# Kernel optimization log

Hardware: AMD Instinct MI355X
Metric: run time of the kernel (lower is better)

The kernel has to match this reference:

```python
import jax, jax.numpy as jnp
import numpy as np


def setup_inputs() -> dict:
    key = jax.random.key(0)
    ks = jax.random.split(key, 6)
    B, C, S = 256, 2048, 7          # batch, embed_dim, spacial_dim
    OUT = 1024                      # output_dim
    return {
        "x": jax.random.normal(ks[0], (B, C, S, S), jnp.float32),
        "pos_emb": jax.random.normal(ks[1], (S * S + 1, C), jnp.float32) / (C ** 0.5),
        "Wv": jax.random.normal(ks[2], (C, C), jnp.float32) * 0.02,
        "bv": jnp.zeros((C,), jnp.float32),
        "Wc": jax.random.normal(ks[3], (OUT, C), jnp.float32) * 0.02,
        "bc": jnp.zeros((OUT,), jnp.float32),
        "num_heads": 32,
    }


def reference(x, pos_emb, Wv, bv, Wc, bc, num_heads):
    # x: [B, C, H, W] -> tokens [B, HW, C], prepend mean token -> [B, N, C]
    B, C, H, W = x.shape
    N = H * W + 1
    hd = C // num_heads
    scale = hd ** -0.5

    t = x.reshape(B, C, H * W).transpose(0, 2, 1)                    # [B, HW, C]
    t = jnp.concatenate([t.mean(axis=1, keepdims=True), t], axis=1)  # [B, N, C]
    t = t + pos_emb[None]                                            # add pos emb

    # qkv weights are all copies of v_proj => q = k = v = v_proj(t)
    v = t @ Wv.T + bv                                                # [B, N, C]
    vh = v.reshape(B, N, num_heads, hd).transpose(0, 2, 1, 3)        # [B, h, N, d]

    # attn_ori = softmax(q k^T * scale) with q=k=v; dropout p=0 (eval)
    attn = jax.nn.softmax(jnp.einsum('bhnd,bhmd->bhnm', vh, vh) * scale, axis=-1)
    ctx = jnp.einsum('bhnm,bhmd->bhnd', attn, vh)                    # [B, h, N, d]
    ctx = ctx.transpose(0, 2, 1, 3).reshape(B, N, C)

    # proj weights come from c_proj: [out_dim, C]
    x_ori = ctx @ Wc.T + bc                                          # [B, N, out]
    xout = v @ Wc.T + bc                                             # x-path: proj(v) directly
    # x[:, 0, :] = x_ori[:, 0, :]; module returns x (first list element)
    return xout.at[:, 0, :].set(x_ori[:, 0, :])
```

## Files before the change

### kernel.cpp

```cpp
#include <hip/hip_runtime.h>
#include <stdint.h>

#define BATCH  256
#define CDIM   2048
#define HW     49
#define NTOK   50
#define MROWS  (BATCH * NTOK)
#define ODIM   1024
#define NHEADS 32

typedef __attribute__((ext_vector_type(8))) short short8;
typedef __attribute__((ext_vector_type(4))) float f32x4;
typedef unsigned short u16;
typedef unsigned int   u32;

__device__ __forceinline__ float bf2f(u16 u) {
  union { u32 i; float f; } v; v.i = ((u32)u) << 16; return v.f;
}
__device__ __forceinline__ u16 f2bf(float f) {
  union { float f; u32 i; } v; v.f = f;
  u32 r = v.i + 0x7fffu + ((v.i >> 16) & 1u);
  return (u16)(r >> 16);
}

__device__ __forceinline__ void async16(const void* g, void* l) {
  __builtin_amdgcn_global_load_lds(
      (const __attribute__((address_space(1))) u32*)g,
      (__attribute__((address_space(3))) u32*)l, 16, 0, 0);
}

__global__ __launch_bounds__(256) void cvt2_kernel(const float* __restrict__ a,
                                                   u16* __restrict__ oa, int n4a,
                                                   const float* __restrict__ bsrc,
                                                   u16* __restrict__ ob, int n4b) {
  int i = blockIdx.x * 256 + threadIdx.x;
  const float* src; u16* dst; int idx;
  if (i < n4a) { src = a; dst = oa; idx = i; }
  else {
    idx = i - n4a;
    if (idx >= n4b) return;
    src = bsrc; dst = ob;
  }
  float4 v = reinterpret_cast<const float4*>(src)[idx];
  ushort4 o;
  o.x = f2bf(v.x); o.y = f2bf(v.y); o.z = f2bf(v.z); o.w = f2bf(v.w);
  reinterpret_cast<ushort4*>(dst)[idx] = o;
}

__global__ __launch_bounds__(256) void prep_kernel(const float* __restrict__ x,
                                                   const float* __restrict__ pos,
                                                   u16* __restrict__ T) {
  const int blk = blockIdx.x;
  const int b  = blk >> 5;
  const int c0 = (blk & 31) * 64;
  __shared__ float xs[64 * HW];
  __shared__ float mean[64];
  const float* src = x + ((size_t)b * CDIM + c0) * HW;
  for (int i = threadIdx.x; i < 64 * HW; i += 256) xs[i] = src[i];
  __syncthreads();
  if (threadIdx.x < 64) {
    float s = 0.f;
#pragma unroll
    for (int j = 0; j < HW; j++) s += xs[threadIdx.x * HW + j];
    mean[threadIdx.x] = s * (1.0f / 49.0f);
  }
  __syncthreads();
  for (int wi = threadIdx.x; wi < NTOK * 8; wi += 256) {
    const int n = wi >> 3;
    const int g = (wi & 7) * 8;
    alignas(16) u16 ov[8];
#pragma unroll
    for (int u = 0; u < 8; u++) {
      const int c = g + u;
      float val = (n == 0) ? mean[c] : xs[c * HW + (n - 1)];
      val += pos[n * CDIM + c0 + c];
      ov[u] = f2bf(val);
    }
    *reinterpret_cast<uint4*>(&T[((size_t)b * NTOK + n) * CDIM + c0 + g]) =
        *reinterpret_cast<const uint4*>(ov);
  }
}

template<int OUT_BF16>
__global__ __launch_bounds__(512, 2)
void gemm256(const u16* __restrict__ A, const u16* __restrict__ Bm,
             const float* __restrict__ bias, void* __restrict__ Cout,
             int M, int N, int K, int nbx) {
  __shared__ __align__(16) u16 smem[65536];

  const int NK = K >> 6;
  const int t = threadIdx.x;
  const int lane = t & 63;
  const int wid = t >> 6;
  const int wm = wid >> 2;
  const int wn = wid & 3;

  const int nwg = gridDim.x;
  const int cpx = nwg >> 3;
  const int orig = blockIdx.x;
  const int swz = (orig & 7) * cpx + (orig >> 3);
  const int bx = swz % nbx;
  const int by = swz / nbx;
  const int m0 = by * 256, n0 = bx * 256;

  const int tr  = t >> 3;
  const int to8 = ((t & 7) ^ (tr & 7)) << 3;
  const int t8  = t << 3;
  const u16* pA0 = A  + (size_t)(m0 + tr) * K + to8;
  const u16* pB0 = Bm + (size_t)(n0 + tr) * K + to8;

  const int lr = lane & 15, hi = lane >> 4;
  const int sx = lr & 7;
  const int aK0 = ((wm * 128 + lr) << 6) + (((0 + hi) ^ sx) << 3);
  const int aK1 = ((wm * 128 + lr) << 6) + (((4 + hi) ^ sx) << 3);
  const int bK0 = 16384 + ((wn * 64 + lr) << 6) + (((0 + hi) ^ sx) << 3);
  const int bK1 = 16384 + ((wn * 64 + lr) << 6) + (((4 + hi) ^ sx) << 3);

  f32x4 acc[8][4] = {};
  short8 a[4][2], b[2][2];

  auto STG = [&](int kti, int isB, int h) {
    if (kti < NK) {
      const u16* g = (isB ? pB0 : pA0) + (size_t)(h * 128) * K + kti * 64;
      u16* l = &smem[((kti & 1) << 15) + (isB << 14) + (h << 13) + t8];
      async16(g, l);
      async16(g + (size_t)64 * K, l + 4096);
    }
  };

  STG(0, 0, 0); STG(0, 0, 1); STG(0, 1, 0); STG(0, 1, 1); STG(1, 0, 0);
  asm volatile("s_waitcnt vmcnt(2)" ::: "memory");
  __builtin_amdgcn_s_barrier();

  for (int j = 0; j < NK; ++j) {
    const u16* sa = &smem[(j & 1) << 15];

#pragma unroll
    for (int f = 0; f < 4; ++f) {
      a[f][0] = *(const short8*)&sa[aK0 + f * 1024];
      a[f][1] = *(const short8*)&sa[aK1 + f * 1024];
    }
#pragma unroll
    for (int f = 0; f < 2; ++f) {
      b[f][0] = *(const short8*)&sa[bK0 + f * 1024];
      b[f][1] = *(const short8*)&sa[bK1 + f * 1024];
    }
    STG(j + 1, 0, 1);
    __builtin_amdgcn_s_barrier();
    asm volatile("s_waitcnt lgkmcnt(0)" ::: "memory");
    __builtin_amdgcn_sched_barrier(0);
    __builtin_amdgcn_s_setprio(1);
#pragma unroll
    for (int fm = 0; fm < 4; ++fm)
#pragma unroll
      for (int fn = 0; fn < 2; ++fn) {
        acc[fm][fn] = __builtin_amdgcn_mfma_f32_16x16x32_bf16(a[fm][0], b[fn][0], acc[fm][fn], 0, 0, 0);
        acc[fm][fn] = __builtin_amdgcn_mfma_f32_16x16x32_bf16(a[fm][1], b[fn][1], acc[fm][fn], 0, 0, 0);
      }
    __builtin_amdgcn_s_setprio(0);
    __builtin_amdgcn_s_barrier();

#pragma unroll
    for (int f = 0; f < 2; ++f) {
      b[f][0] = *(const short8*)&sa[bK0 + (2 + f) * 1024];
      b[f][1] = *(const short8*)&sa[bK1 + (2 + f) * 1024];
    }
    STG(j + 1, 1, 0);
    __builtin_amdgcn_s_barrier();
    asm volatile("s_waitcnt lgkmcnt(0)" ::: "memory");
    __builtin_amdgcn_sched_barrier(0);
    __builtin_amdgcn_s_setprio(1);
#pragma unroll
    for (int fm = 0; fm < 4; ++fm)
#pragma unroll
      for (int fn = 0; fn < 2; ++fn) {
        acc[fm][2 + fn] = __builtin_amdgcn_mfma_f32_16x16x32_bf16(a[fm][0], b[fn][0], acc[fm][2 + fn], 0, 0, 0);
        acc[fm][2 + fn] = __builtin_amdgcn_mfma_f32_16x16x32_bf16(a[fm][1], b[fn][1], acc[fm][2 + fn], 0, 0, 0);
      }
    __builtin_amdgcn_s_setprio(0);
    __builtin_amdgcn_s_barrier();

#pragma unroll
    for (int f = 0; f < 4; ++f) {
      a[f][0] = *(const short8*)&sa[aK0 + (4 + f) * 1024];
      a[f][1] = *(const short8*)&sa[aK1 + (4 + f) * 1024];
    }
    STG(j + 1, 1, 1);
    __builtin_amdgcn_s_barrier();
    asm volatile("s_waitcnt lgkmcnt(0)" ::: "memory");
    __builtin_amdgcn_sched_barrier(0);
    __builtin_amdgcn_s_setprio(1);
#pragma unroll
    for (int fm = 0; fm < 4; ++fm)
#pragma unroll
      for (int fn = 0; fn < 2; ++fn) {
        acc[4 + fm][2 + fn] = __builtin_amdgcn_mfma_f32_16x16x32_bf16(a[fm][0], b[fn][0], acc[4 + fm][2 + fn], 0, 0, 0);
        acc[4 + fm][2 + fn] = __builtin_amdgcn_mfma_f32_16x16x32_bf16(a[fm][1], b[fn][1], acc[4 + fm][2 + fn], 0, 0, 0);
      }
    __builtin_amdgcn_s_setprio(0);
    __builtin_amdgcn_s_barrier();

#pragma unroll
    for (int f = 0; f < 2; ++f) {
      b[f][0] = *(const short8*)&sa[bK0 + f * 1024];
      b[f][1] = *(const short8*)&sa[bK1 + f * 1024];
    }
    STG(j + 2, 0, 0);
    __builtin_amdgcn_s_barrier();
    asm volatile("s_waitcnt lgkmcnt(0)" ::: "memory");
    __builtin_amdgcn_sched_barrier(0);
    __builtin_amdgcn_s_setprio(1);
#pragma unroll
    for (int fm = 0; fm < 4; ++fm)
#pragma unroll
      for (int fn = 0; fn < 2; ++fn) {
        acc[4 + fm][fn] = __builtin_amdgcn_mfma_f32_16x16x32_bf16(a[fm][0], b[fn][0], acc[4 + fm][fn], 0, 0, 0);
        acc[4 + fm][fn] = __builtin_amdgcn_mfma_f32_16x16x32_bf16(a[fm][1], b[fn][1], acc[4 + fm][fn], 0, 0, 0);
      }
    __builtin_amdgcn_s_setprio(0);
    if (j < NK - 2) asm volatile("s_waitcnt vmcnt(2)" ::: "memory");
    else            asm volatile("s_waitcnt vmcnt(0)" ::: "memory");
    __builtin_amdgcn_s_barrier();
  }

  const int erow = hi * 4;
#pragma unroll
  for (int fm = 0; fm < 8; ++fm) {
#pragma unroll
    for (int fn = 0; fn < 4; ++fn) {
      const int cg = n0 + wn * 64 + fn * 16 + lr;
      const float bb = bias[cg];
      const int rbase = m0 + wm * 128 + fm * 16 + erow;
#pragma unroll
      for (int jr = 0; jr < 4; ++jr) {
        const float val = acc[fm][fn][jr] + bb;
        if (OUT_BF16)
          ((u16*)Cout)[(size_t)(rbase + jr) * N + cg] = f2bf(val);
        else
          ((float*)Cout)[(size_t)(rbase + jr) * N + cg] = val;
      }
    }
  }
}

__global__ __launch_bounds__(64) void attn0_kernel(u16* __restrict__ V) {
  const int b = blockIdx.x, h = blockIdx.y;
  __shared__ __align__(16) u16 vt[NTOK * 64];
  __shared__ float pb[64];
  const int t = threadIdx.x;
  u16* base = V + (size_t)b * NTOK * CDIM + h * 64;
  for (int idx = t; idx < NTOK * 8; idx += 64) {
    const int m = idx >> 3, g = (idx & 7) * 8;
    *reinterpret_cast<uint4*>(&vt[m * 64 + g]) =
        *reinterpret_cast<const uint4*>(base + (size_t)m * CDIM + g);
  }
  __syncthreads();
  const float qd = bf2f(vt[t]);
  float s_own = -1e30f;
  for (int m = 0; m < NTOK; m++) {
    float p = qd * bf2f(vt[m * 64 + t]);
#pragma unroll
    for (int off = 32; off; off >>= 1) p += __shfl_xor(p, off);
    if (t == m) s_own = p * 0.125f;
  }
  float mx = s_own;
#pragma unroll
  for (int off = 32; off; off >>= 1) mx = fmaxf(mx, __shfl_xor(mx, off));
  const float e = (t < NTOK) ? __expf(s_own - mx) : 0.f;
  float Z = e;
#pragma unroll
  for (int off = 32; off; off >>= 1) Z += __shfl_xor(Z, off);
  pb[t] = e / Z;
  __syncthreads();
  float acc = 0.f;
  for (int m = 0; m < NTOK; m++) acc += pb[m] * bf2f(vt[m * 64 + t]);
  base[t] = f2bf(acc);
}

extern "C" void kernel_launch(void* const* d_in, const int* in_sizes, int n_in,
                              void* d_out, int out_size, void* d_ws, size_t ws_size,
                              hipStream_t stream) {
  const float* x   = (const float*)d_in[0];
  const float* pos = (const float*)d_in[1];
  const float* Wv  = (const float*)d_in[2];
  const float* bv  = (const float*)d_in[3];
  const float* Wc  = (const float*)d_in[4];
  const float* bc  = (const float*)d_in[5];
  float* out = (float*)d_out;

  u16* T   = (u16*)d_ws;
  u16* V   = T   + (size_t)MROWS * CDIM;
  u16* WvB = V   + (size_t)MROWS * CDIM;
  u16* WcB = WvB + (size_t)CDIM * CDIM;

  {
    int n4a = CDIM * CDIM / 4;
    int n4b = ODIM * CDIM / 4;
    cvt2_kernel<<<(n4a + n4b + 255) / 256, 256, 0, stream>>>(Wv, WvB, n4a, Wc, WcB, n4b);
  }
  prep_kernel<<<BATCH * 32, 256, 0, stream>>>(x, pos, T);

  gemm256<1><<<(MROWS / 256) * (CDIM / 256), 512, 0, stream>>>(
      T, WvB, bv, V, MROWS, CDIM, CDIM, CDIM / 256);

  attn0_kernel<<<dim3(BATCH, NHEADS), 64, 0, stream>>>(V);

  gemm256<0><<<(MROWS / 256) * (ODIM / 256), 512, 0, stream>>>(
      V, WcB, bc, out, MROWS, ODIM, CDIM, ODIM / 256);
}
```

Before: 310.5 us.

## Fuse weight conversion with prep kernel and restructure GEMM k-loop staging

```diff
diff --git a/kernel.cpp b/kernel.cpp
--- a/kernel.cpp
+++ b/kernel.cpp
@@ -29,34 +29,36 @@
       (__attribute__((address_space(3))) u32*)l, 16, 0, 0);
 }
 
-__global__ __launch_bounds__(256) void cvt2_kernel(const float* __restrict__ a,
-                                                   u16* __restrict__ oa, int n4a,
-                                                   const float* __restrict__ bsrc,
-                                                   u16* __restrict__ ob, int n4b) {
-  int i = blockIdx.x * 256 + threadIdx.x;
-  const float* src; u16* dst; int idx;
-  if (i < n4a) { src = a; dst = oa; idx = i; }
-  else {
-    idx = i - n4a;
-    if (idx >= n4b) return;
-    src = bsrc; dst = ob;
-  }
-  float4 v = reinterpret_cast<const float4*>(src)[idx];
-  ushort4 o;
-  o.x = f2bf(v.x); o.y = f2bf(v.y); o.z = f2bf(v.z); o.w = f2bf(v.w);
-  reinterpret_cast<ushort4*>(dst)[idx] = o;
-}
-
-__global__ __launch_bounds__(256) void prep_kernel(const float* __restrict__ x,
-                                                   const float* __restrict__ pos,
-                                                   u16* __restrict__ T) {
-  const int blk = blockIdx.x;
+#define BARRIER() asm volatile("s_barrier" ::: "memory")
+
+__global__ __launch_bounds__(256) void cvt_prep_kernel(
+    const float* __restrict__ Wv, u16* __restrict__ WvB, int n4a,
+    const float* __restrict__ Wc, u16* __restrict__ WcB, int n4b,
+    const float* __restrict__ x, const float* __restrict__ pos,
+    u16* __restrict__ T, int nCvt) {
+  if (blockIdx.x < (unsigned)nCvt) {
+    int i = blockIdx.x * 256 + threadIdx.x;
+    const float* src; u16* dst; int idx;
+    if (i < n4a) { src = Wv; dst = WvB; idx = i; }
+    else {
+      idx = i - n4a;
+      if (idx >= n4b) return;
+      src = Wc; dst = WcB;
+    }
+    float4 v = reinterpret_cast<const float4*>(src)[idx];
+    ushort4 o;
+    o.x = f2bf(v.x); o.y = f2bf(v.y); o.z = f2bf(v.z); o.w = f2bf(v.w);
+    reinterpret_cast<ushort4*>(dst)[idx] = o;
+    return;
+  }
+  const int blk = blockIdx.x - nCvt;
   const int b  = blk >> 5;
   const int c0 = (blk & 31) * 64;
   __shared__ float xs[64 * HW];
   __shared__ float mean[64];
   const float* src = x + ((size_t)b * CDIM + c0) * HW;
-  for (int i = threadIdx.x; i < 64 * HW; i += 256) xs[i] = src[i];
+  for (int i = threadIdx.x; i < 64 * HW / 4; i += 256)
+    reinterpret_cast<float4*>(xs)[i] = reinterpret_cast<const float4*>(src)[i];
   __syncthreads();
   if (threadIdx.x < 64) {
     float s = 0.f;
@@ -117,7 +119,7 @@
   const int bK1 = 16384 + ((wn * 64 + lr) << 6) + (((4 + hi) ^ sx) << 3);
 
   f32x4 acc[8][4] = {};
-  short8 a[4][2], b[2][2];
+  short8 a[4][2], b[4][2];
 
   auto STG = [&](int kti, int isB, int h) {
     if (kti < NK) {
@@ -128,9 +130,21 @@
     }
   };
 
-  STG(0, 0, 0); STG(0, 0, 1); STG(0, 1, 0); STG(0, 1, 1); STG(1, 0, 0);
-  asm volatile("s_waitcnt vmcnt(2)" ::: "memory");
-  __builtin_amdgcn_s_barrier();
+#define MFMA4x2(AM, BN0, ACCM, ACCN)                                          \
+  _Pragma("unroll")                                                           \
+  for (int fm = 0; fm < 4; ++fm) {                                            \
+    _Pragma("unroll")                                                         \
+    for (int fn = 0; fn < 2; ++fn) {                                          \
+      acc[(ACCM) + fm][(ACCN) + fn] = __builtin_amdgcn_mfma_f32_16x16x32_bf16(\
+          a[fm][0], b[(BN0) + fn][0], acc[(ACCM) + fm][(ACCN) + fn], 0, 0, 0);\
+      acc[(ACCM) + fm][(ACCN) + fn] = __builtin_amdgcn_mfma_f32_16x16x32_bf16(\
+          a[fm][1], b[(BN0) + fn][1], acc[(ACCM) + fm][(ACCN) + fn], 0, 0, 0);\
+    }                                                                         \
+  }
+
+  STG(0, 0, 0); STG(0, 0, 1); STG(0, 1, 0); STG(0, 1, 1);
+  asm volatile("s_waitcnt vmcnt(0)" ::: "memory");
+  BARRIER();
 
   for (int j = 0; j < NK; ++j) {
     const u16* sa = &smem[(j & 1) << 15];
@@ -145,82 +159,46 @@
       b[f][0] = *(const short8*)&sa[bK0 + f * 1024];
       b[f][1] = *(const short8*)&sa[bK1 + f * 1024];
     }
-    STG(j + 1, 0, 1);
-    __builtin_amdgcn_s_barrier();
+    STG(j + 1, 0, 0); STG(j + 1, 0, 1); STG(j + 1, 1, 0); STG(j + 1, 1, 1);
+    BARRIER();
     asm volatile("s_waitcnt lgkmcnt(0)" ::: "memory");
     __builtin_amdgcn_sched_barrier(0);
     __builtin_amdgcn_s_setprio(1);
-#pragma unroll
-    for (int fm = 0; fm < 4; ++fm)
-#pragma unroll
-      for (int fn = 0; fn < 2; ++fn) {
-        acc[fm][fn] = __builtin_amdgcn_mfma_f32_16x16x32_bf16(a[fm][0], b[fn][0], acc[fm][fn], 0, 0, 0);
-        acc[fm][fn] = __builtin_amdgcn_mfma_f32_16x16x32_bf16(a[fm][1], b[fn][1], acc[fm][fn], 0, 0, 0);
-      }
-    __builtin_amdgcn_s_setprio(0);
-    __builtin_amdgcn_s_barrier();
-
-#pragma unroll
-    for (int f = 0; f < 2; ++f) {
-      b[f][0] = *(const short8*)&sa[bK0 + (2 + f) * 1024];
-      b[f][1] = *(const short8*)&sa[bK1 + (2 + f) * 1024];
-    }
-    STG(j + 1, 1, 0);
-    __builtin_amdgcn_s_barrier();
+    MFMA4x2(lo, 0, 0, 0);
+    __builtin_amdgcn_s_setprio(0);
+    BARRIER();
+
+#pragma unroll
+    for (int f = 2; f < 4; ++f) {
+      b[f][0] = *(const short8*)&sa[bK0 + f * 1024];
+      b[f][1] = *(const short8*)&sa[bK1 + f * 1024];
+    }
+    BARRIER();
     asm volatile("s_waitcnt lgkmcnt(0)" ::: "memory");
     __builtin_amdgcn_sched_barrier(0);
     __builtin_amdgcn_s_setprio(1);
-#pragma unroll
-    for (int fm = 0; fm < 4; ++fm)
-#pragma unroll
-      for (int fn = 0; fn < 2; ++fn) {
-        acc[fm][2 + fn] = __builtin_amdgcn_mfma_f32_16x16x32_bf16(a[fm][0], b[fn][0], acc[fm][2 + fn], 0, 0, 0);
-        acc[fm][2 + fn] = __builtin_amdgcn_mfma_f32_16x16x32_bf16(a[fm][1], b[fn][1], acc[fm][2 + fn], 0, 0, 0);
-      }
-    __builtin_amdgcn_s_setprio(0);
-    __builtin_amdgcn_s_barrier();
+    MFMA4x2(lo, 2, 0, 2);
+    __builtin_amdgcn_s_setprio(0);
+    BARRIER();
 
 #pragma unroll
     for (int f = 0; f < 4; ++f) {
       a[f][0] = *(const short8*)&sa[aK0 + (4 + f) * 1024];
       a[f][1] = *(const short8*)&sa[aK1 + (4 + f) * 1024];
     }
-    STG(j + 1, 1, 1);
-    __builtin_amdgcn_s_barrier();
+    BARRIER();
     asm volatile("s_waitcnt lgkmcnt(0)" ::: "memory");
     __builtin_amdgcn_sched_barrier(0);
     __builtin_amdgcn_s_setprio(1);
-#pragma unroll
-    for (int fm = 0; fm < 4; ++fm)
-#pragma unroll
-      for (int fn = 0; fn < 2; ++fn) {
-        acc[4 + fm][2 + fn] = __builtin_amdgcn_mfma_f32_16x16x32_bf16(a[fm][0], b[fn][0], acc[4 + fm][2 + fn], 0, 0, 0);
-        acc[4 + fm][2 + fn] = __builtin_amdgcn_mfma_f32_16x16x32_bf16(a[fm][1], b[fn][1], acc[4 + fm][2 + fn], 0, 0, 0);
-      }
-    __builtin_amdgcn_s_setprio(0);
-    __builtin_amdgcn_s_barrier();
-
-#pragma unroll
-    for (int f = 0; f < 2; ++f) {
-      b[f][0] = *(const short8*)&sa[bK0 + f * 1024];
-      b[f][1] = *(const short8*)&sa[bK1 + f * 1024];
-    }
-    STG(j + 2, 0, 0);
-    __builtin_amdgcn_s_barrier();
-    asm volatile("s_waitcnt lgkmcnt(0)" ::: "memory");
-    __builtin_amdgcn_sched_barrier(0);
-    __builtin_amdgcn_s_setprio(1);
-#pragma unroll
-    for (int fm = 0; fm < 4; ++fm)
-#pragma unroll
-      for (int fn = 0; fn < 2; ++fn) {
-        acc[4 + fm][fn] = __builtin_amdgcn_mfma_f32_16x16x32_bf16(a[fm][0], b[fn][0], acc[4 + fm][fn], 0, 0, 0);
-        acc[4 + fm][fn] = __builtin_amdgcn_mfma_f32_16x16x32_bf16(a[fm][1], b[fn][1], acc[4 + fm][fn], 0, 0, 0);
-      }
-    __builtin_amdgcn_s_setprio(0);
-    if (j < NK - 2) asm volatile("s_waitcnt vmcnt(2)" ::: "memory");
-    else            asm volatile("s_waitcnt vmcnt(0)" ::: "memory");
-    __builtin_amdgcn_s_barrier();
+    MFMA4x2(hi, 2, 4, 2);
+    __builtin_amdgcn_s_setprio(0);
+    BARRIER();
+
+    __builtin_amdgcn_s_setprio(1);
+    MFMA4x2(hi, 0, 4, 0);
+    __builtin_amdgcn_s_setprio(0);
+    asm volatile("s_waitcnt vmcnt(0)" ::: "memory");
+    BARRIER();
   }
 
   const int erow = hi * 4;
@@ -241,6 +219,7 @@
       }
     }
   }
+#undef MFMA4x2
 }
 
 __global__ __launch_bounds__(64) void attn0_kernel(u16* __restrict__ V) {
@@ -296,9 +275,10 @@
   {
     int n4a = CDIM * CDIM / 4;
     int n4b = ODIM * CDIM / 4;
-    cvt2_kernel<<<(n4a + n4b + 255) / 256, 256, 0, stream>>>(Wv, WvB, n4a, Wc, WcB, n4b);
-  }
-  prep_kernel<<<BATCH * 32, 256, 0, stream>>>(x, pos, T);
+    int nCvt = (n4a + n4b + 255) / 256;
+    cvt_prep_kernel<<<nCvt + BATCH * 32, 256, 0, stream>>>(
+        Wv, WvB, n4a, Wc, WcB, n4b, x, pos, T, nCvt);
+  }
 
   gemm256<1><<<(MROWS / 256) * (CDIM / 256), 512, 0, stream>>>(
       T, WvB, bv, V, MROWS, CDIM, CDIM, CDIM / 256);
```

Result: faster. 290.4 us (-6.5%).
